# Performance work log

Hardware: AMD Instinct MI355X
Metric: run time of the kernel (lower is better)

Reference implementation:

```python
import jax, jax.numpy as jnp
import numpy as np

EPS = 1e-8
STRIDE = 1
PADDING = 1  # init_kwargs padding


def setup_inputs() -> dict:
    key = jax.random.key(0)
    k1, k2, k3, k4 = jax.random.split(key, 4)
    B, IC, OC, DL, K, H, W = 16, 256, 256, 512, 3, 64, 64
    return {
        "image": jax.random.normal(k1, (B, IC, H, W), dtype=jnp.float32),
        "style": jax.random.normal(k2, (B, DL), dtype=jnp.float32),
        "weight": jax.random.normal(k3, (OC, IC, K, K), dtype=jnp.float32),
        "mod_weight": jax.random.normal(k4, (IC, DL), dtype=jnp.float32),
    }


def reference(image, style, weight, mod_weight):
    B, IC, H, W = image.shape
    OC, _, K, _ = weight.shape
    DL = mod_weight.shape[1]

    # WeightScaledLinear: style -> per-input-channel modulation scale s [B, IC]
    mod_scale = np.sqrt(2.0 / DL).astype(np.float32)
    s = style @ (mod_weight * mod_scale).T  # [B, IC]

    # Conv weight equalized-lr scale
    w_scale = np.sqrt(2.0 / (IC * K * K)).astype(np.float32)

    # Demodulation uses the UNSCALED base weight (faithful to source):
    # rsqrt(sum_{ic,kh,kw} weight^2 + eps), per output channel [OC]
    demod = jax.lax.rsqrt(jnp.sum(weight * weight, axis=(1, 2, 3)) + EPS)

    # Per-sample modulated conv == scale input channels by s, then shared conv,
    # then scale output channels by demod. This folds the groups=batch trick
    # into a single batched conv (identical math).
    x = image * s[:, :, None, None]  # [B, IC, H, W]
    out = jax.lax.conv_general_dilated(
        x, weight * w_scale,
        window_strides=(STRIDE, STRIDE),
        padding=[(PADDING, PADDING), (PADDING, PADDING)],
        dimension_numbers=("NCHW", "OIHW", "NCHW"),
    )  # [B, OC, H, W]
    return out * demod[None, :, None, None]
```

## Files before the change

### kernel.cpp

```cpp
#include <hip/hip_runtime.h>

typedef __bf16 bf16x8 __attribute__((ext_vector_type(8)));
typedef float  f32x4  __attribute__((ext_vector_type(4)));

#define IC    256
#define OC    256
#define Hh    64
#define Ww    64
#define Bb    16
#define DLEN  512
#define KKTOT 2304
#define HP    66
#define MODSCALE 0.0625f
#define WSCALE   0.029462782549439484f

#define XT_ELEMS  (Bb*HP*HP*IC)
#define XT_BYTES  (XT_ELEMS*2)
#define WMAT_OFF  XT_BYTES
#define WMAT_BYTES (OC*KKTOT*2)
#define S_OFF     (WMAT_OFF + WMAT_BYTES)

typedef const __attribute__((address_space(1))) unsigned int* gptr_t;
typedef __attribute__((address_space(3))) unsigned int* lptr_t;

__device__ __forceinline__ void gl2lds16(const void* g, void* l) {
  __builtin_amdgcn_global_load_lds((gptr_t)g, (lptr_t)l, 16, 0, 0);
}

#define BARRIER()    __builtin_amdgcn_s_barrier()
#define WAIT_VM4()   asm volatile("s_waitcnt vmcnt(4)" ::: "memory")
#define WAIT_VM0()   asm volatile("s_waitcnt vmcnt(0)" ::: "memory")

__global__ void k_style(const float* __restrict__ style,
                        const float* __restrict__ mw,
                        float* __restrict__ s_out) {
  __shared__ float st[DLEN];
  const int b = blockIdx.x, t = threadIdx.x;
  st[t]       = style[b*DLEN + t];
  st[t + 256] = style[b*DLEN + t + 256];
  __syncthreads();
  const float4* mwr = (const float4*)(mw + (long)t*DLEN);
  float acc = 0.f;
  #pragma unroll 4
  for (int d = 0; d < DLEN/4; ++d) {
    float4 v = mwr[d];
    acc += v.x*st[d*4] + v.y*st[d*4+1] + v.z*st[d*4+2] + v.w*st[d*4+3];
  }
  s_out[b*IC + t] = acc * MODSCALE;
}

__global__ void k_wmat(const float* __restrict__ wt, __bf16* __restrict__ wmat) {
  const int oc = blockIdx.x, t = threadIdx.x;
  float w9[9];
  const float* p = wt + ((long)oc*IC + t)*9;
  float ss = 0.f;
  #pragma unroll
  for (int r = 0; r < 9; ++r) { w9[r] = p[r]; ss += w9[r]*w9[r]; }
  #pragma unroll
  for (int off = 32; off; off >>= 1) ss += __shfl_down(ss, off, 64);
  __shared__ float red[4];
  if ((t & 63) == 0) red[t >> 6] = ss;
  __syncthreads();
  float total = red[0] + red[1] + red[2] + red[3];
  float dm = WSCALE / sqrtf(total + 1e-8f);
  #pragma unroll
  for (int r = 0; r < 9; ++r)
    wmat[oc*KKTOT + r*IC + t] = (__bf16)(w9[r] * dm);
}

__global__ void k_halo(__bf16* __restrict__ xt) {
  const int b = blockIdx.x, t = threadIdx.x;
  uint4* base = (uint4*)(xt + (long)b*HP*HP*IC);
  const uint4 z = {0u,0u,0u,0u};
  for (int i = t; i < 2112; i += 256) { base[i] = z; base[137280 + i] = z; }
  for (int i = t; i < 64*32; i += 256) {
    int y = 1 + (i >> 5), c = i & 31;
    base[y*2112 + c] = z;
    base[y*2112 + 2080 + c] = z;
  }
}

__global__ void k_xmod(const float* __restrict__ img,
                       const float* __restrict__ s,
                       __bf16* __restrict__ xt) {
  __shared__ float tile[64][69];
  const int t   = threadIdx.x;
  const int b   = blockIdx.x >> 8;
  const int rem = blockIdx.x & 255;
  const int y   = rem >> 2;
  const int ic0 = (rem & 3) << 6;
  #pragma unroll
  for (int r = 0; r < 4; ++r) {
    int seg = r*256 + t;
    int i   = seg >> 4;
    int x0  = (seg & 15) * 4;
    float4 v = *(const float4*)(img + (((long)(b*IC + ic0 + i)*Hh + y)*Ww + x0));
    float sv = s[b*IC + ic0 + i];
    tile[i][x0+0] = v.x*sv; tile[i][x0+1] = v.y*sv;
    tile[i][x0+2] = v.z*sv; tile[i][x0+3] = v.w*sv;
  }
  __syncthreads();
  const int x  = t >> 2;
  const int j0 = (t & 3) << 4;
  bf16x8 o0, o1;
  #pragma unroll
  for (int e = 0; e < 8; ++e) o0[e] = (__bf16)tile[j0 + e][x];
  #pragma unroll
  for (int e = 0; e < 8; ++e) o1[e] = (__bf16)tile[j0 + 8 + e][x];
  __bf16* dst = xt + (((long)(b*HP + y + 1)*HP + (x + 1))*IC + ic0 + j0);
  ((bf16x8*)dst)[0] = o0;
  ((bf16x8*)dst)[1] = o1;
}

__global__ __launch_bounds__(512, 2) void k_conv(const __bf16* __restrict__ wmat,
                                                 const __bf16* __restrict__ xt,
                                                 float* __restrict__ out) {
  __shared__ __attribute__((aligned(128))) char ldsc[131072];
  const int tid  = threadIdx.x;
  const int lane = tid & 63;
  const int wv   = tid >> 6;
  const int wr   = wv >> 2;
  const int wc   = wv & 3;

  const int bi     = blockIdx.x;
  const int b      = ((bi & 7) << 1) | ((bi >> 7) & 1);
  const int hwBase = ((bi >> 3) & 15) << 8;

  const int row0 = tid >> 3;
  const int c8   = (tid & 7) ^ (row0 & 7);
  const long aOff0 = (long)row0*KKTOT + c8*8;
  const long aOff1 = aOff0 + (long)64*KKTOT;
  const int x  = row0;
  const int y0 = hwBase >> 6;
  long bOff[2][2];
  #pragma unroll
  for (int h = 0; h < 2; ++h)
    #pragma unroll
    for (int l = 0; l < 2; ++l)
      bOff[h][l] = (((long)b*HP + y0 + 2*h + l)*HP + x)*IC + c8*8;
  const unsigned wvOff = wv << 10;

#define STAGE_A(tt, h) do {                                              \
    char* d_ = ldsc + (((tt)&1)<<16) + ((h)<<14) + wvOff;                \
    const __bf16* g_ = wmat + (h)*(128*KKTOT) + (tt)*64;                 \
    gl2lds16(g_ + aOff0, d_);                                            \
    gl2lds16(g_ + aOff1, d_ + 8192);                                     \
  } while (0)

#define STAGE_B(tt, h, sb) do {                                          \
    char* d_ = ldsc + (((tt)&1)<<16) + 32768 + ((h)<<14) + wvOff;        \
    gl2lds16(xt + bOff[h][0] + (sb), d_);                                \
    gl2lds16(xt + bOff[h][1] + (sb), d_ + 8192);                         \
  } while (0)

  STAGE_A(0, 0); STAGE_A(0, 1);
  STAGE_B(0, 0, 0);  STAGE_B(0, 1, 0);
  STAGE_B(1, 0, 64); STAGE_B(1, 1, 64);
  WAIT_VM4();
  BARRIER();

  f32x4 acc[8][4] = {};
  bf16x8 af[2][2][2];
  bf16x8 bfr[4][2];
  const int cb = (lane >> 4) << 4;
  const int rA = wr*128 + (lane & 15);
  const int rB = wc*64  + (lane & 15);

#define READ_A(set, q) do {                                              \
    _Pragma("unroll")                                                    \
    for (int m2 = 0; m2 < 2; ++m2) {                                     \
      int rr = rA + (q)*32 + m2*16, sw = (rr & 7) << 4;                  \
      af[set][m2][0] = *(const bf16x8*)(Abuf + rr*128 + ((  0 + cb) ^ sw)); \
      af[set][m2][1] = *(const bf16x8*)(Abuf + rr*128 + (( 64 + cb) ^ sw)); \
    }                                                                    \
  } while (0)

#define MFMA_Q(set, q) do {                                              \
    __builtin_amdgcn_s_setprio(1);                                       \
    _Pragma("unroll")                                                    \
    for (int m2 = 0; m2 < 2; ++m2)                                       \
      _Pragma("unroll")                                                  \
      for (int n = 0; n < 4; ++n) {                                      \
        acc[(q)*2+m2][n] = __builtin_amdgcn_mfma_f32_16x16x32_bf16(af[set][m2][0], bfr[n][0], acc[(q)*2+m2][n], 0, 0, 0); \
        acc[(q)*2+m2][n] = __builtin_amdgcn_mfma_f32_16x16x32_bf16(af[set][m2][1], bfr[n][1], acc[(q)*2+m2][n], 0, 0, 0); \
      }                                                                  \
    __builtin_amdgcn_s_setprio(0);                                       \
  } while (0)

  for (int t = 0; t < 36; ++t) {
    char* Abuf = ldsc + ((t & 1) << 16);
    char* Bbuf = Abuf + 32768;
    int sbB = 0;
    if (t < 34) {
      int tt = t + 2, pos = tt >> 2, kh = pos/3;
      sbB = (kh*HP + (pos - kh*3))*IC + ((tt & 3) << 6);
    }

    READ_A(0, 0);
    #pragma unroll
    for (int n = 0; n < 4; ++n) {
      int rr = rB + n*16, sw = (rr & 7) << 4;
      bfr[n][0] = *(const bf16x8*)(Bbuf + rr*128 + ((  0 + cb) ^ sw));
      bfr[n][1] = *(const bf16x8*)(Bbuf + rr*128 + (( 64 + cb) ^ sw));
    }
    READ_A(1, 1);
    if (t < 35) STAGE_A(t+1, 0);
    BARRIER();
    MFMA_Q(0, 0);
    BARRIER();

    READ_A(0, 2);
    if (t < 35) STAGE_A(t+1, 1);
    BARRIER();
    MFMA_Q(1, 1);
    BARRIER();

    READ_A(1, 3);
    if (t < 34) STAGE_B(t+2, 0, sbB);
    BARRIER();
    MFMA_Q(0, 2);
    BARRIER();

    if (t < 34) STAGE_B(t+2, 1, sbB);
    BARRIER();
    MFMA_Q(1, 3);
    if (t >= 34) { WAIT_VM0(); } else { WAIT_VM4(); }
    BARRIER();
  }

  float* outb = out + (((long)b*OC + wr*128 + ((lane >> 4) << 2))*(Hh*Ww))
                    + hwBase + wc*64 + (lane & 15);
  #pragma unroll
  for (int m = 0; m < 8; ++m)
    #pragma unroll
    for (int n = 0; n < 4; ++n)
      #pragma unroll
      for (int j = 0; j < 4; ++j)
        outb[((long)(m*16 + j))*(Hh*Ww) + n*16] = acc[m][n][j];
}

extern "C" void kernel_launch(void* const* d_in, const int* in_sizes, int n_in,
                              void* d_out, int out_size, void* d_ws, size_t ws_size,
                              hipStream_t stream) {
  const float* image = (const float*)d_in[0];
  const float* style = (const float*)d_in[1];
  const float* weight= (const float*)d_in[2];
  const float* modw  = (const float*)d_in[3];
  float* out = (float*)d_out;

  char* ws = (char*)d_ws;
  __bf16* xt   = (__bf16*)ws;
  __bf16* wmat = (__bf16*)(ws + WMAT_OFF);
  float*  sbuf = (float*)(ws + S_OFF);

  k_style<<<Bb, 256, 0, stream>>>(style, modw, sbuf);
  k_wmat<<<OC, 256, 0, stream>>>(weight, wmat);
  k_halo<<<Bb, 256, 0, stream>>>(xt);
  k_xmod<<<Bb*64*4, 256, 0, stream>>>(image, sbuf, xt);
  k_conv<<<256, 512, 0, stream>>>(wmat, xt, out);
}
```

Before: 113.5 us.

## Simplify conv GEMM pipeline to single-stage prefetch with one barrier per tile

Replaces the hand-scheduled pipeline, which interleaved explicit barriers, vmcnt waits and a two-tile-ahead B prefetch, with a simpler scheme. Both A and B for the next K-tile are now staged during the first half of the current tile, and there is one __syncthreads per iteration. The A-fragment register set is halved and the MFMA loop is reordered by k-slice. This cuts barrier count and register pressure, but global loads now have less lead time, so load latency is less hidden.

```diff
diff --git a/kernel.cpp b/kernel.cpp
--- a/kernel.cpp
+++ b/kernel.cpp
@@ -27,10 +27,6 @@
   __builtin_amdgcn_global_load_lds((gptr_t)g, (lptr_t)l, 16, 0, 0);
 }
 
-#define BARRIER()    __builtin_amdgcn_s_barrier()
-#define WAIT_VM4()   asm volatile("s_waitcnt vmcnt(4)" ::: "memory")
-#define WAIT_VM0()   asm volatile("s_waitcnt vmcnt(0)" ::: "memory")
-
 __global__ void k_style(const float* __restrict__ style,
                         const float* __restrict__ mw,
                         float* __restrict__ s_out) {
@@ -154,78 +150,63 @@
   } while (0)
 
   STAGE_A(0, 0); STAGE_A(0, 1);
-  STAGE_B(0, 0, 0);  STAGE_B(0, 1, 0);
-  STAGE_B(1, 0, 64); STAGE_B(1, 1, 64);
-  WAIT_VM4();
-  BARRIER();
+  STAGE_B(0, 0, 0); STAGE_B(0, 1, 0);
+  __syncthreads();
 
   f32x4 acc[8][4] = {};
-  bf16x8 af[2][2][2];
+  bf16x8 af[2][2];
   bf16x8 bfr[4][2];
   const int cb = (lane >> 4) << 4;
   const int rA = wr*128 + (lane & 15);
   const int rB = wc*64  + (lane & 15);
 
-#define READ_A(set, q) do {                                              \
+#define READ_A(q) do {                                                   \
     _Pragma("unroll")                                                    \
     for (int m2 = 0; m2 < 2; ++m2) {                                     \
       int rr = rA + (q)*32 + m2*16, sw = (rr & 7) << 4;                  \
-      af[set][m2][0] = *(const bf16x8*)(Abuf + rr*128 + ((  0 + cb) ^ sw)); \
-      af[set][m2][1] = *(const bf16x8*)(Abuf + rr*128 + (( 64 + cb) ^ sw)); \
+      af[m2][0] = *(const bf16x8*)(Abuf + rr*128 + ((  0 + cb) ^ sw));   \
+      af[m2][1] = *(const bf16x8*)(Abuf + rr*128 + (( 64 + cb) ^ sw));   \
     }                                                                    \
   } while (0)
 
-#define MFMA_Q(set, q) do {                                              \
+#define MFMA_Q(q) do {                                                   \
     __builtin_amdgcn_s_setprio(1);                                       \
     _Pragma("unroll")                                                    \
-    for (int m2 = 0; m2 < 2; ++m2)                                       \
+    for (int ks = 0; ks < 2; ++ks)                                       \
       _Pragma("unroll")                                                  \
-      for (int n = 0; n < 4; ++n) {                                      \
-        acc[(q)*2+m2][n] = __builtin_amdgcn_mfma_f32_16x16x32_bf16(af[set][m2][0], bfr[n][0], acc[(q)*2+m2][n], 0, 0, 0); \
-        acc[(q)*2+m2][n] = __builtin_amdgcn_mfma_f32_16x16x32_bf16(af[set][m2][1], bfr[n][1], acc[(q)*2+m2][n], 0, 0, 0); \
-      }                                                                  \
+      for (int m2 = 0; m2 < 2; ++m2)                                     \
+        _Pragma("unroll")                                                \
+        for (int n = 0; n < 4; ++n)                                      \
+          acc[(q)*2+m2][n] = __builtin_amdgcn_mfma_f32_16x16x32_bf16(af[m2][ks], bfr[n][ks], acc[(q)*2+m2][n], 0, 0, 0); \
     __builtin_amdgcn_s_setprio(0);                                       \
   } while (0)
 
   for (int t = 0; t < 36; ++t) {
     char* Abuf = ldsc + ((t & 1) << 16);
     char* Bbuf = Abuf + 32768;
-    int sbB = 0;
-    if (t < 34) {
-      int tt = t + 2, pos = tt >> 2, kh = pos/3;
-      sbB = (kh*HP + (pos - kh*3))*IC + ((tt & 3) << 6);
-    }
-
-    READ_A(0, 0);
+    const int tt = t + 1, pos = tt >> 2, kh = pos/3;
+    const int sb1 = (kh*HP + (pos - kh*3))*IC + ((tt & 3) << 6);
+
     #pragma unroll
     for (int n = 0; n < 4; ++n) {
       int rr = rB + n*16, sw = (rr & 7) << 4;
       bfr[n][0] = *(const bf16x8*)(Bbuf + rr*128 + ((  0 + cb) ^ sw));
       bfr[n][1] = *(const bf16x8*)(Bbuf + rr*128 + (( 64 + cb) ^ sw));
     }
-    READ_A(1, 1);
-    if (t < 35) STAGE_A(t+1, 0);
-    BARRIER();
-    MFMA_Q(0, 0);
-    BARRIER();
-
-    READ_A(0, 2);
-    if (t < 35) STAGE_A(t+1, 1);
-    BARRIER();
-    MFMA_Q(1, 1);
-    BARRIER();
-
-    READ_A(1, 3);
-    if (t < 34) STAGE_B(t+2, 0, sbB);
-    BARRIER();
-    MFMA_Q(0, 2);
-    BARRIER();
-
-    if (t < 34) STAGE_B(t+2, 1, sbB);
-    BARRIER();
-    MFMA_Q(1, 3);
-    if (t >= 34) { WAIT_VM0(); } else { WAIT_VM4(); }
-    BARRIER();
+    READ_A(0);
+    if (t < 35) { STAGE_A(tt, 0); STAGE_B(tt, 0, sb1); }
+    MFMA_Q(0);
+
+    READ_A(1);
+    if (t < 35) { STAGE_A(tt, 1); STAGE_B(tt, 1, sb1); }
+    MFMA_Q(1);
+
+    READ_A(2);
+    MFMA_Q(2);
+    READ_A(3);
+    MFMA_Q(3);
+
+    __syncthreads();
   }
 
   float* outb = out + (((long)b*OC + wr*128 + ((lane >> 4) << 2))*(Hh*Ww))
```

New measurement: 108.7 us. 4.2% less time.
